# Kernel tuning notes

Measured on AMD Instinct MI355X. Metric: run time of the kernel, lower is better.

The kernel has to match this reference:

```python
import jax, jax.numpy as jnp
import numpy as np

DIM = 512
HEADS = 8
DH = DIM // HEADS  # 64

def setup_inputs() -> dict:
    key = jax.random.key(0)
    ks = jax.random.split(key, 10)
    s = 1.0 / np.sqrt(DIM)
    return {
        "x": jax.random.normal(ks[0], (8, 4096, DIM), dtype=jnp.float32),
        "x_d": jax.random.normal(ks[1], (8, 4096, DIM), dtype=jnp.float32),
        "W_qkv_rgb": jax.random.normal(ks[2], (DIM, 3 * DIM), dtype=jnp.float32) * s,
        "W_qkv_T": jax.random.normal(ks[3], (DIM, 3 * DIM), dtype=jnp.float32) * s,
        "temperature_rgb": jnp.ones((HEADS, 1, 1), dtype=jnp.float32),
        "temperature_T": jnp.ones((HEADS, 1, 1), dtype=jnp.float32),
        "W_proj_rgb": jax.random.normal(ks[4], (DIM, DIM), dtype=jnp.float32) * s,
        "b_proj_rgb": jnp.zeros((DIM,), dtype=jnp.float32),
        "W_proj_T": jax.random.normal(ks[5], (DIM, DIM), dtype=jnp.float32) * s,
        "b_proj_T": jnp.zeros((DIM,), dtype=jnp.float32),
    }

def _split_qkv(t, W):
    # t: (B,N,C) -> q,k,v each (B,H,d,N)  (channels-as-tokens layout)
    B, N, C = t.shape
    qkv = (t @ W).reshape(B, N, 3, HEADS, DH)
    qkv = qkv.transpose(2, 0, 3, 4, 1)  # (3,B,H,d,N)
    return qkv[0], qkv[1], qkv[2]

def _l2norm(a):
    # normalize over last axis (token dim N), matching F.normalize eps=1e-12
    n = jnp.sqrt(jnp.sum(a * a, axis=-1, keepdims=True))
    return a / jnp.maximum(n, 1e-12)

def _xca(q, k, v, temp):
    # q,k,v: (B,H,d,N); temp: (H,1,1) -> out (B,N,C)
    attn = jnp.einsum("bhdn,bhen->bhde", q, k) * temp  # (B,H,d,d)
    attn = jax.nn.softmax(attn, axis=-1)
    out = jnp.einsum("bhde,bhen->bhdn", attn, v)  # (B,H,d,N)
    B = out.shape[0]
    N = out.shape[-1]
    return out.transpose(0, 3, 1, 2).reshape(B, N, HEADS * DH)

def reference(x, x_d, W_qkv_rgb, W_qkv_T, temperature_rgb, temperature_T,
              W_proj_rgb, b_proj_rgb, W_proj_T, b_proj_T):
    q_rgb, k_rgb, v_rgb = _split_qkv(x, W_qkv_rgb)
    q_T, k_T, v_T = _split_qkv(x_d, W_qkv_T)
    q_rgb = _l2norm(q_rgb); k_rgb = _l2norm(k_rgb)
    q_T = _l2norm(q_T); k_T = _l2norm(k_T)
    out_rgb = _xca(q_rgb, k_T, v_T, temperature_rgb)
    out_T = _xca(q_T, k_rgb, v_rgb, temperature_T)
    out_rgb = out_rgb @ W_proj_rgb + b_proj_rgb
    out_T = out_T @ W_proj_T + b_proj_T
    return out_rgb, out_T
```

## Files before the change

kernel.cpp:

```cpp
#include <hip/hip_runtime.h>
#include <hip/hip_bf16.h>
#include <math.h>
#include <stdint.h>

typedef __bf16 bf16;
typedef __bf16 bf16x8 __attribute__((ext_vector_type(8)));
typedef float  floatx4 __attribute__((ext_vector_type(4)));

#define HEADS 8
#define DH    64
#define NB    8
#define NTOK  4096
#define CDIM  512
#define MTOT  32768
#define PART_STRIDE 16777216L

__device__ __forceinline__ void gload16(const bf16* g, bf16* l) {
    __builtin_amdgcn_global_load_lds(
        (const __attribute__((address_space(1))) unsigned int*)g,
        (__attribute__((address_space(3))) unsigned int*)l,
        16, 0, 0);
}

__global__ void detect_kernel(const bf16* __restrict__ w, int* __restrict__ flag)
{
    __shared__ int cnt[256];
    int c = 0;
    for (int i = 0; i < 64; ++i) {
        float v = fabsf((float)w[threadIdx.x + i * 256]);
        if (v > 1e3f) c++;
    }
    cnt[threadIdx.x] = c;
    __syncthreads();
    if (threadIdx.x == 0) {
        int s = 0;
        for (int i = 0; i < 256; ++i) s += cnt[i];
        *flag = (s > 500) ? 1 : 0;
    }
}

__global__ void misc_kernel(const void* t0, const void* t1, const void* b0, const void* b1,
                            const int* __restrict__ flag, float* __restrict__ misc)
{
    bool f32 = (*flag != 0);
    int tid = threadIdx.x;
    #define RD(p, i) (f32 ? ((const float*)(p))[i] : (float)((const bf16*)(p))[i])
    if (tid < 8) { misc[tid] = RD(t0, tid); misc[8 + tid] = RD(t1, tid); }
    for (int i = tid; i < 512; i += 256) {
        misc[16 + i]  = RD(b0, i);
        misc[528 + i] = RD(b1, i);
    }
    #undef RD
}

__global__ void wt_kernel(const void* __restrict__ W, bf16* __restrict__ Wt, int K, int N,
                          const int* __restrict__ flag)
{
    int idx = blockIdx.x * 256 + threadIdx.x;
    if (idx >= K * N) return;
    bool f32 = (*flag != 0);
    int n = idx / K;
    int k = idx - n * K;
    float v = f32 ? ((const float*)W)[k * N + n] : (float)((const bf16*)W)[k * N + n];
    Wt[idx] = (bf16)v;
}

__global__ void cast_kernel(const void* __restrict__ X, bf16* __restrict__ Y,
                            const int* __restrict__ flag)
{
    size_t i = ((size_t)blockIdx.x * 256 + threadIdx.x) * 8;
    if (*flag) {
        const float* xf = (const float*)X + i;
        float4 a = *(const float4*)xf;
        float4 b = *(const float4*)(xf + 4);
        bf16 t[8] = {(bf16)a.x, (bf16)a.y, (bf16)a.z, (bf16)a.w,
                     (bf16)b.x, (bf16)b.y, (bf16)b.z, (bf16)b.w};
        *(uint4*)(Y + i) = *(uint4*)t;
    } else {
        *(uint4*)(Y + i) = *(const uint4*)((const bf16*)X + i);
    }
}

__global__ __launch_bounds__(512, 2) void gemm_bt(
    const bf16* __restrict__ A, const bf16* __restrict__ Bt,
    const float* __restrict__ bias, void* __restrict__ C, bf16* __restrict__ Cv,
    long c_base, const int* __restrict__ cflag)
{
    __shared__ bf16 lds[2][2][2][128 * 64];

    const int tid  = threadIdx.x;
    const int lane = tid & 63;
    const int w    = tid >> 6;
    const int wmi  = w >> 2;
    const int wni  = w & 3;
    const int l15  = lane & 15;
    const int quad = lane >> 4;

    const int m0 = blockIdx.x * 256;
    const int n0 = blockIdx.y * 256;

    const int rl0 = w * 16 + (lane >> 3);
    const int swz = ((lane & 7) ^ (rl0 & 7)) * 8;
    const bf16* Abase = A  + (size_t)(m0 + rl0) * 512 + swz;
    const bf16* Bbase = Bt + (size_t)(n0 + rl0) * 512 + swz;
    const int ldst0 = w * 1024;

    const int rxor  = l15 & 7;
    const int k0off = (quad ^ rxor) * 8;
    const int k1off = ((4 + quad) ^ rxor) * 8;
    const bf16* Ah0 = &lds[0][0][wmi][l15 * 64];
    const bf16* Ah1 = &lds[1][0][wmi][l15 * 64];
    const bf16* Bh0 = &lds[0][1][wni >> 1][((wni & 1) * 64 + l15) * 64];
    const bf16* Bh1 = &lds[1][1][wni >> 1][((wni & 1) * 64 + l15) * 64];

    bf16x8 aR[4][2], bR[4][2];
    floatx4 acc[8][4] = {};

#define STAGE_A(b, h, t) do { \
    const bf16* _g = Abase + (h) * 65536 + (t) * 64; \
    gload16(_g,        &lds[b][0][h][ldst0]); \
    gload16(_g + 4096, &lds[b][0][h][ldst0 + 512]); \
} while (0)
#define STAGE_B(b, h, t) do { \
    const bf16* _g = Bbase + (h) * 65536 + (t) * 64; \
    gload16(_g,        &lds[b][1][h][ldst0]); \
    gload16(_g + 4096, &lds[b][1][h][ldst0 + 512]); \
} while (0)
#define RD_A(b, qm) do { \
    _Pragma("unroll") for (int _i = 0; _i < 4; ++_i) { \
        aR[_i][0] = *(const bf16x8*)(Ah##b + ((qm) * 4 + _i) * 1024 + k0off); \
        aR[_i][1] = *(const bf16x8*)(Ah##b + ((qm) * 4 + _i) * 1024 + k1off); \
    } \
} while (0)
#define RD_B(b, qn) do { \
    _Pragma("unroll") for (int _j = 0; _j < 2; ++_j) { \
        bR[(qn) * 2 + _j][0] = *(const bf16x8*)(Bh##b + ((qn) * 2 + _j) * 1024 + k0off); \
        bR[(qn) * 2 + _j][1] = *(const bf16x8*)(Bh##b + ((qn) * 2 + _j) * 1024 + k1off); \
    } \
} while (0)
#define MM(qm, qn) do { \
    _Pragma("unroll") for (int _i = 0; _i < 4; ++_i) \
    _Pragma("unroll") for (int _j = 0; _j < 2; ++_j) { \
        acc[(qm)*4+_i][(qn)*2+_j] = __builtin_amdgcn_mfma_f32_16x16x32_bf16( \
            aR[_i][0], bR[(qn)*2+_j][0], acc[(qm)*4+_i][(qn)*2+_j], 0, 0, 0); \
        acc[(qm)*4+_i][(qn)*2+_j] = __builtin_amdgcn_mfma_f32_16x16x32_bf16( \
            aR[_i][1], bR[(qn)*2+_j][1], acc[(qm)*4+_i][(qn)*2+_j], 0, 0, 0); \
    } \
} while (0)
#define SYNC   asm volatile("s_barrier" ::: "memory")
#define VMW(n) asm volatile("s_waitcnt vmcnt(" #n ")" ::: "memory")
#define PRIO1  __builtin_amdgcn_s_setprio(1)
#define PRIO0  __builtin_amdgcn_s_setprio(0)

#define TILE(t, b, nb, W) do { \
     \
    RD_A(b, 0); RD_B(b, 0); \
    if ((t) + 1 < 8) STAGE_B(nb, 1, (t) + 1); \
    SYNC; PRIO1; MM(0, 0); PRIO0; SYNC; \
     \
    RD_B(b, 1); \
    if ((t) + 1 < 8) STAGE_A(nb, 1, (t) + 1); \
    SYNC; PRIO1; MM(0, 1); PRIO0; SYNC; \
     \
    RD_A(b, 1); \
    if ((t) + 2 < 8) STAGE_B(b, 0, (t) + 2); \
    SYNC; PRIO1; MM(1, 1); PRIO0; SYNC; \
     \
    if ((t) + 2 < 8) STAGE_A(b, 0, (t) + 2); \
    SYNC; PRIO1; MM(1, 0); PRIO0; \
    VMW(W); SYNC; \
} while (0)

    STAGE_A(0, 0, 0); STAGE_A(0, 1, 0); STAGE_B(0, 0, 0); STAGE_B(0, 1, 0);
    STAGE_B(1, 0, 1); STAGE_A(1, 0, 1);
    VMW(4);
    SYNC;

    TILE(0, 0, 1, 4);
    TILE(1, 1, 0, 4);
    TILE(2, 0, 1, 4);
    TILE(3, 1, 0, 4);
    TILE(4, 0, 1, 4);
    TILE(5, 1, 0, 4);
    TILE(6, 0, 1, 0);
    TILE(7, 1, 0, 0);

#undef TILE
#undef STAGE_A
#undef STAGE_B
#undef RD_A
#undef RD_B
#undef MM
#undef SYNC
#undef VMW
#undef PRIO1
#undef PRIO0

    const bool cf32 = cflag && (*cflag != 0);
    const int  part = n0 >> 9;
    const long rowB = (long)m0 + wmi * 128 + quad * 4;
    const int  colB = (n0 & 511) + wni * 64 + l15;

    float bv[4];
    #pragma unroll
    for (int fj = 0; fj < 4; ++fj)
        bv[fj] = bias ? bias[n0 + wni * 64 + fj * 16 + l15] : 0.0f;

    if (part == 2) {
        #pragma unroll
        for (int fi = 0; fi < 8; ++fi)
            #pragma unroll
            for (int rr = 0; rr < 4; ++rr) {
                bf16* op = Cv + (rowB + fi * 16 + rr) * CDIM + colB;
                #pragma unroll
                for (int fj = 0; fj < 4; ++fj)
                    op[fj * 16] = (bf16)acc[fi][fj][rr];
            }
    } else if (cf32) {
        float* Cp = (float*)C + c_base + (long)part * PART_STRIDE;
        #pragma unroll
        for (int fi = 0; fi < 8; ++fi)
            #pragma unroll
            for (int rr = 0; rr < 4; ++rr) {
                float* op = Cp + (rowB + fi * 16 + rr) * CDIM + colB;
                #pragma unroll
                for (int fj = 0; fj < 4; ++fj)
                    op[fj * 16] = acc[fi][fj][rr] + bv[fj];
            }
    } else {
        bf16* Cp = (bf16*)C + c_base + (long)part * PART_STRIDE;
        #pragma unroll
        for (int fi = 0; fi < 8; ++fi)
            #pragma unroll
            for (int rr = 0; rr < 4; ++rr) {
                bf16* op = Cp + (rowB + fi * 16 + rr) * CDIM + colB;
                #pragma unroll
                for (int fj = 0; fj < 4; ++fj)
                    op[fj * 16] = (bf16)(acc[fi][fj][rr] + bv[fj]);
            }
    }
}

__global__ __launch_bounds__(256) void xca_gk(
    const bf16* __restrict__ Q0, const bf16* __restrict__ K0,
    const bf16* __restrict__ Q1, const bf16* __restrict__ K1,
    float* __restrict__ G, float* __restrict__ NQ, float* __restrict__ NK)
{
    __shared__ bf16 Tq[64 * 72];
    __shared__ bf16 Tk[64 * 72];

    int bid = blockIdx.x;
    int nq4 = bid & 3;
    int h   = (bid >> 2) & 7;
    int b   = (bid >> 5) & 7;
    int s   = bid >> 8;
    int sbh = s * 64 + b * 8 + h;

    const bf16* qsrc = s ? Q1 : Q0;
    const bf16* ksrc = s ? K0 : K1;

    int tid  = threadIdx.x;
    int lane = tid & 63;
    int wv   = tid >> 6;
    int wr   = wv >> 1;
    int wc   = wv & 1;
    int l15  = lane & 15;
    int quad = lane >> 4;
    bool isQ = (wv == 0 || wv == 3);

    int m_thr = tid & 7;
    int d0    = m_thr * 8;
    int u     = tid >> 3;
    int u_w   = u ^ (m_thr << 2);
    int wbase = d0 * 72 + 2 * u_w;

    int aoff[2][2], boff[2][2];
    #pragma unroll
    for (int i = 0; i < 2; ++i) {
        int ra = wr * 32 + i * 16 + l15;
        int rb = wc * 32 + i * 16 + l15;
        #pragma unroll
        for (int ss = 0; ss < 2; ++ss) {
            int ulog = ss * 16 + quad * 4;
            aoff[i][ss] = ra * 72 + 2 * (ulog ^ ((ra >> 3) << 2));
            boff[i][ss] = rb * 72 + 2 * (ulog ^ ((rb >> 3) << 2));
        }
    }

    long gbase = (long)(b * NTOK + nq4 * 1024) * CDIM + h * DH + d0;
    const bf16* qg = qsrc + gbase;
    const bf16* kg = ksrc + gbase;

    floatx4 accG[2][2] = {};
    floatx4 accN[2] = {};

    uint4 qA, qB, kA, kB;
    {
        size_t off = (size_t)(2 * u) * CDIM;
        qA = *(const uint4*)(qg + off);
        qB = *(const uint4*)(qg + off + CDIM);
        kA = *(const uint4*)(kg + off);
        kB = *(const uint4*)(kg + off + CDIM);
    }

    for (int t = 0; t < 16; ++t) {
        __syncthreads();
        {
            const unsigned short* pa = (const unsigned short*)&qA;
            const unsigned short* pb = (const unsigned short*)&qB;
            const unsigned short* pc = (const unsigned short*)&kA;
            const unsigned short* pd = (const unsigned short*)&kB;
            #pragma unroll
            for (int j = 0; j < 8; ++j) {
                *(uint32_t*)((char*)Tq + (size_t)(wbase + j * 72) * 2) =
                    (uint32_t)pa[j] | ((uint32_t)pb[j] << 16);
                *(uint32_t*)((char*)Tk + (size_t)(wbase + j * 72) * 2) =
                    (uint32_t)pc[j] | ((uint32_t)pd[j] << 16);
            }
        }
        __syncthreads();
        if (t + 1 < 16) {
            size_t off = (size_t)((t + 1) * 64 + 2 * u) * CDIM;
            qA = *(const uint4*)(qg + off);
            qB = *(const uint4*)(qg + off + CDIM);
            kA = *(const uint4*)(kg + off);
            kB = *(const uint4*)(kg + off + CDIM);
        }
        #pragma unroll
        for (int ss = 0; ss < 2; ++ss) {
            bf16x8 a0 = *(const bf16x8*)&Tq[aoff[0][ss]];
            bf16x8 a1 = *(const bf16x8*)&Tq[aoff[1][ss]];
            bf16x8 b0 = *(const bf16x8*)&Tk[boff[0][ss]];
            bf16x8 b1 = *(const bf16x8*)&Tk[boff[1][ss]];
            accG[0][0] = __builtin_amdgcn_mfma_f32_16x16x32_bf16(a0, b0, accG[0][0], 0, 0, 0);
            accG[0][1] = __builtin_amdgcn_mfma_f32_16x16x32_bf16(a0, b1, accG[0][1], 0, 0, 0);
            accG[1][0] = __builtin_amdgcn_mfma_f32_16x16x32_bf16(a1, b0, accG[1][0], 0, 0, 0);
            accG[1][1] = __builtin_amdgcn_mfma_f32_16x16x32_bf16(a1, b1, accG[1][1], 0, 0, 0);
            if (isQ) {
                accN[0] = __builtin_amdgcn_mfma_f32_16x16x32_bf16(a0, a0, accN[0], 0, 0, 0);
                accN[1] = __builtin_amdgcn_mfma_f32_16x16x32_bf16(a1, a1, accN[1], 0, 0, 0);
            } else {
                accN[0] = __builtin_amdgcn_mfma_f32_16x16x32_bf16(b0, b0, accN[0], 0, 0, 0);
                accN[1] = __builtin_amdgcn_mfma_f32_16x16x32_bf16(b1, b1, accN[1], 0, 0, 0);
            }
        }
    }

    float* Gp = G + (size_t)sbh * 4096;
    #pragma unroll
    for (int i = 0; i < 2; ++i)
        #pragma unroll
        for (int j = 0; j < 2; ++j)
            #pragma unroll
            for (int rr = 0; rr < 4; ++rr)
                atomicAdd(&Gp[(wr * 32 + i * 16 + quad * 4 + rr) * 64 + wc * 32 + j * 16 + l15],
                          accG[i][j][rr]);

    float* Np  = isQ ? NQ : NK;
    int nbase  = (isQ ? wr : wc) * 32;
    if ((l15 >> 2) == quad) {
        atomicAdd(&Np[(size_t)sbh * 64 + nbase + l15],      accN[0][l15 & 3]);
        atomicAdd(&Np[(size_t)sbh * 64 + nbase + 16 + l15], accN[1][l15 & 3]);
    }
}

__global__ void xca_soft(const float* __restrict__ G,
                         const float* __restrict__ NQ, const float* __restrict__ NK,
                         const float* __restrict__ misc, bf16* __restrict__ P)
{
    int sbh = blockIdx.x;
    int s = sbh >> 6;
    int h = sbh & 7;
    int d = threadIdx.x;

    __shared__ float rk[64];
    rk[d] = 1.0f / fmaxf(sqrtf(NK[sbh * 64 + d]), 1e-12f);
    __syncthreads();

    float rq = 1.0f / fmaxf(sqrtf(NQ[sbh * 64 + d]), 1e-12f);
    float t  = misc[s * 8 + h];
    const float* Gr = G + (sbh * 64 + d) * 64;

    float a[64];
    float mx = -1e30f;
    #pragma unroll
    for (int e = 0; e < 64; ++e) {
        a[e] = Gr[e] * rq * rk[e] * t;
        mx = fmaxf(mx, a[e]);
    }
    float sum = 0.f;
    #pragma unroll
    for (int e = 0; e < 64; ++e) { a[e] = expf(a[e] - mx); sum += a[e]; }
    float inv = 1.0f / sum;
    bf16* Pr = P + (sbh * 64 + d) * 64;
    #pragma unroll
    for (int e = 0; e < 64; ++e) Pr[e] = (bf16)(a[e] * inv);
}

__global__ __launch_bounds__(256) void xca_pv(
    const bf16* __restrict__ V0, const bf16* __restrict__ V1,
    const bf16* __restrict__ P, bf16* __restrict__ xca)
{
    int bid = blockIdx.x;
    int nq4 = bid & 3;
    int h   = (bid >> 2) & 7;
    int b   = (bid >> 5) & 7;
    int s   = bid >> 8;
    int sbh = s * 64 + b * 8 + h;

    const bf16* vsrc = s ? V0 : V1;

    int tid = threadIdx.x;
    int lane = tid & 63;
    int wave = tid >> 6;
    int l15 = lane & 15;
    int quad = lane >> 4;

    const bf16* Pb = P + sbh * 4096;
    bf16x8 pf[4][2];
    #pragma unroll
    for (int i = 0; i < 4; ++i)
        #pragma unroll
        for (int h2 = 0; h2 < 2; ++h2)
            pf[i][h2] = *(const bf16x8*)&Pb[(i * 16 + l15) * 64 + h2 * 32 + quad * 8];

    int n_start = nq4 * 1024 + wave * 256;
    for (int nt = 0; nt < 16; ++nt) {
        int nb = n_start + nt * 16;
        const bf16* vp = vsrc + (long)(b * NTOK + nb + l15) * CDIM + h * DH + quad * 8;
        bf16x8 v0 = *(const bf16x8*)vp;
        bf16x8 v1 = *(const bf16x8*)(vp + 32);
        floatx4 acc[4] = {};
        #pragma unroll
        for (int i = 0; i < 4; ++i) {
            acc[i] = __builtin_amdgcn_mfma_f32_16x16x32_bf16(v0, pf[i][0], acc[i], 0, 0, 0);
            acc[i] = __builtin_amdgcn_mfma_f32_16x16x32_bf16(v1, pf[i][1], acc[i], 0, 0, 0);
        }
        bf16* op = xca + (long)((s * NB + b) * NTOK + nb + quad * 4) * CDIM + h * DH + l15;
        #pragma unroll
        for (int i = 0; i < 4; ++i)
            #pragma unroll
            for (int r = 0; r < 4; ++r)
                op[(long)r * CDIM + i * 16] = (bf16)acc[i][r];
    }
}

extern "C" void kernel_launch(void* const* d_in, const int* in_sizes, int n_in,
                              void* d_out, int out_size, void* d_ws, size_t ws_size,
                              hipStream_t stream)
{
    const void* x     = d_in[0];
    const void* x_d   = d_in[1];
    const void* Wq0   = d_in[2];
    const void* Wq1   = d_in[3];
    const void* temp0 = d_in[4];
    const void* temp1 = d_in[5];
    const void* Wp0   = d_in[6];
    const void* bp0   = d_in[7];
    const void* Wp1   = d_in[8];
    const void* bp1   = d_in[9];

    char* ws = (char*)d_ws;
    bf16*  Q0   = (bf16*)(ws);
    bf16*  K0   = (bf16*)(ws + 33554432);
    bf16*  Q1   = (bf16*)(ws + 67108864);
    bf16*  K1   = (bf16*)(ws + 100663296);
    bf16*  Xb0  = (bf16*)(ws + 134217728);
    bf16*  Xb1  = (bf16*)(ws + 167772160);
    bf16*  xca  = (bf16*)(ws + 134217728);
    bf16*  wtq0 = (bf16*)(ws + 201326592);
    bf16*  wtq1 = (bf16*)(ws + 202899456);
    bf16*  wtp0 = (bf16*)(ws + 204472320);
    bf16*  wtp1 = (bf16*)(ws + 204996608);
    float* G    = (float*)(ws + 205520896);
    float* NQ   = (float*)(ws + 207618048);
    float* NK   = (float*)(ws + 207650816);
    bf16*  P    = (bf16*)(ws + 207683584);
    int*   flag = (int*)(ws + 208732160);
    float* misc = (float*)(ws + 208732224);

    bf16* V0 = (bf16*)d_out;
    bf16* V1 = (bf16*)d_out + PART_STRIDE;

    hipMemsetAsync(ws + 205520896, 0, 2162688, stream);

    detect_kernel<<<1, 256, 0, stream>>>((const bf16*)Wq0, flag);
    misc_kernel<<<1, 256, 0, stream>>>(temp0, temp1, bp0, bp1, flag, misc);

    wt_kernel<<<(512 * 1536 + 255) / 256, 256, 0, stream>>>(Wq0, wtq0, 512, 1536, flag);
    wt_kernel<<<(512 * 1536 + 255) / 256, 256, 0, stream>>>(Wq1, wtq1, 512, 1536, flag);
    wt_kernel<<<(512 * 512 + 255) / 256, 256, 0, stream>>>(Wp0, wtp0, 512, 512, flag);
    wt_kernel<<<(512 * 512 + 255) / 256, 256, 0, stream>>>(Wp1, wtp1, 512, 512, flag);

    cast_kernel<<<8192, 256, 0, stream>>>(x,   Xb0, flag);
    cast_kernel<<<8192, 256, 0, stream>>>(x_d, Xb1, flag);

    gemm_bt<<<dim3(128, 6), 512, 0, stream>>>(Xb0, wtq0, nullptr, Q0, V0, 0L, nullptr);
    gemm_bt<<<dim3(128, 6), 512, 0, stream>>>(Xb1, wtq1, nullptr, Q1, V1, 0L, nullptr);

    xca_gk<<<512, 256, 0, stream>>>(Q0, K0, Q1, K1, G, NQ, NK);
    xca_soft<<<128, 64, 0, stream>>>(G, NQ, NK, misc, P);
    xca_pv<<<512, 256, 0, stream>>>(V0, V1, P, xca);

    gemm_bt<<<dim3(128, 2), 512, 0, stream>>>(xca,               wtp0, misc + 16,  d_out, nullptr, 0L,          flag);
    gemm_bt<<<dim3(128, 2), 512, 0, stream>>>(xca + PART_STRIDE, wtp1, misc + 528, d_out, nullptr, PART_STRIDE, flag);
}
```

Before: 528.9 us.

## Merge small prep kernels, batch GEMM launches, and stage epilogues through LDS

Folds the weight-transpose and misc kernels into one prep kernel and the two cast launches into one, cutting launch count. Each QKV GEMM launch becomes one z-batched launch in which a block loops over three N-tiles and overlaps the previous tile's epilogue with the next tile's loads. GEMM and PV epilogues now stage results in swizzled LDS so global stores are 16-byte and coalesced instead of scattered 2-byte writes. The trade-offs are fewer blocks in flight for the QKV GEMM, and reuse of the operand-staging LDS as epilogue scratch, which could race if the waits are wrong.

```diff
diff --git a/kernel.cpp b/kernel.cpp
--- a/kernel.cpp
+++ b/kernel.cpp
@@ -39,36 +39,47 @@
     }
 }
 
-__global__ void misc_kernel(const void* t0, const void* t1, const void* b0, const void* b1,
-                            const int* __restrict__ flag, float* __restrict__ misc)
-{
-    bool f32 = (*flag != 0);
-    int tid = threadIdx.x;
-    #define RD(p, i) (f32 ? ((const float*)(p))[i] : (float)((const bf16*)(p))[i])
-    if (tid < 8) { misc[tid] = RD(t0, tid); misc[8 + tid] = RD(t1, tid); }
-    for (int i = tid; i < 512; i += 256) {
-        misc[16 + i]  = RD(b0, i);
-        misc[528 + i] = RD(b1, i);
-    }
-    #undef RD
-}
-
-__global__ void wt_kernel(const void* __restrict__ W, bf16* __restrict__ Wt, int K, int N,
-                          const int* __restrict__ flag)
-{
-    int idx = blockIdx.x * 256 + threadIdx.x;
+__device__ __forceinline__ void wt_body(const void* __restrict__ W, bf16* __restrict__ Wt,
+                                        int K, int N, bool f32, int idx)
+{
     if (idx >= K * N) return;
-    bool f32 = (*flag != 0);
     int n = idx / K;
     int k = idx - n * K;
     float v = f32 ? ((const float*)W)[k * N + n] : (float)((const bf16*)W)[k * N + n];
     Wt[idx] = (bf16)v;
 }
 
-__global__ void cast_kernel(const void* __restrict__ X, bf16* __restrict__ Y,
+__global__ void prep_kernel(const void* Wq0, const void* Wq1, const void* Wp0, const void* Wp1,
+                            const void* t0, const void* t1, const void* b0, const void* b1,
+                            const int* __restrict__ flag, float* __restrict__ misc,
+                            bf16* wtq0, bf16* wtq1, bf16* wtp0, bf16* wtp1)
+{
+    bool f32 = (*flag != 0);
+    int blk = blockIdx.x;
+    int tid = threadIdx.x;
+    if (blk < 3072)      wt_body(Wq0, wtq0, 512, 1536, f32, blk * 256 + tid);
+    else if (blk < 6144) wt_body(Wq1, wtq1, 512, 1536, f32, (blk - 3072) * 256 + tid);
+    else if (blk < 7168) wt_body(Wp0, wtp0, 512, 512, f32, (blk - 6144) * 256 + tid);
+    else if (blk < 8192) wt_body(Wp1, wtp1, 512, 512, f32, (blk - 7168) * 256 + tid);
+    else {
+        #define RD(p, i) (f32 ? ((const float*)(p))[i] : (float)((const bf16*)(p))[i])
+        if (tid < 8) { misc[tid] = RD(t0, tid); misc[8 + tid] = RD(t1, tid); }
+        for (int i = tid; i < 512; i += 256) {
+            misc[16 + i]  = RD(b0, i);
+            misc[528 + i] = RD(b1, i);
+        }
+        #undef RD
+    }
+}
+
+__global__ void cast_kernel(const void* __restrict__ X0, const void* __restrict__ X1,
+                            bf16* __restrict__ Y0, bf16* __restrict__ Y1,
                             const int* __restrict__ flag)
 {
-    size_t i = ((size_t)blockIdx.x * 256 + threadIdx.x) * 8;
+    int blk = blockIdx.x;
+    const void* X = (blk < 8192) ? X0 : X1;
+    bf16* Y       = (blk < 8192) ? Y0 : Y1;
+    size_t i = ((size_t)(blk & 8191) * 256 + threadIdx.x) * 8;
     if (*flag) {
         const float* xf = (const float*)X + i;
         float4 a = *(const float4*)xf;
@@ -81,12 +92,22 @@
     }
 }
 
+template<int NJOBS>
 __global__ __launch_bounds__(512, 2) void gemm_bt(
-    const bf16* __restrict__ A, const bf16* __restrict__ Bt,
-    const float* __restrict__ bias, void* __restrict__ C, bf16* __restrict__ Cv,
-    long c_base, const int* __restrict__ cflag)
+    const bf16* __restrict__ A0, const bf16* __restrict__ A1,
+    const bf16* __restrict__ Bt0, const bf16* __restrict__ Bt1,
+    const float* __restrict__ bias0, const float* __restrict__ bias1,
+    void* __restrict__ C, bf16* __restrict__ Cv0, bf16* __restrict__ Cv1,
+    long cbase0, long cbase1, const int* __restrict__ cflag)
 {
     __shared__ bf16 lds[2][2][2][128 * 64];
+
+    const int z = blockIdx.z;
+    const bf16* A    = z ? A1 : A0;
+    const bf16* Btz  = z ? Bt1 : Bt0;
+    const float* bias = z ? bias1 : bias0;
+    bf16* Cvz        = z ? Cv1 : Cv0;
+    const long c_base = z ? cbase1 : cbase0;
 
     const int tid  = threadIdx.x;
     const int lane = tid & 63;
@@ -97,12 +118,11 @@
     const int quad = lane >> 4;
 
     const int m0 = blockIdx.x * 256;
-    const int n0 = blockIdx.y * 256;
 
     const int rl0 = w * 16 + (lane >> 3);
     const int swz = ((lane & 7) ^ (rl0 & 7)) * 8;
-    const bf16* Abase = A  + (size_t)(m0 + rl0) * 512 + swz;
-    const bf16* Bbase = Bt + (size_t)(n0 + rl0) * 512 + swz;
+    const bf16* Abase = A + (size_t)(m0 + rl0) * 512 + swz;
+    const bf16* Bbase = nullptr;
     const int ldst0 = w * 1024;
 
     const int rxor  = l15 & 7;
@@ -112,6 +132,8 @@
     const bf16* Ah1 = &lds[1][0][wmi][l15 * 64];
     const bf16* Bh0 = &lds[0][1][wni >> 1][((wni & 1) * 64 + l15) * 64];
     const bf16* Bh1 = &lds[1][1][wni >> 1][((wni & 1) * 64 + l15) * 64];
+
+    bf16* eb = (bf16*)lds + ((w < 4) ? (5 * 8192 + w * 2048) : (7 * 8192 + (w - 4) * 2048));
 
     bf16x8 aR[4][2], bR[4][2];
     floatx4 acc[8][4] = {};
@@ -153,37 +175,100 @@
 #define PRIO0  __builtin_amdgcn_s_setprio(0)
 
 #define TILE(t, b, nb, W) do { \
-     \
     RD_A(b, 0); RD_B(b, 0); \
     if ((t) + 1 < 8) STAGE_B(nb, 1, (t) + 1); \
     SYNC; PRIO1; MM(0, 0); PRIO0; SYNC; \
-     \
     RD_B(b, 1); \
     if ((t) + 1 < 8) STAGE_A(nb, 1, (t) + 1); \
     SYNC; PRIO1; MM(0, 1); PRIO0; SYNC; \
-     \
     RD_A(b, 1); \
     if ((t) + 2 < 8) STAGE_B(b, 0, (t) + 2); \
     SYNC; PRIO1; MM(1, 1); PRIO0; SYNC; \
-     \
     if ((t) + 2 < 8) STAGE_A(b, 0, (t) + 2); \
     SYNC; PRIO1; MM(1, 0); PRIO0; \
     VMW(W); SYNC; \
 } while (0)
 
-    STAGE_A(0, 0, 0); STAGE_A(0, 1, 0); STAGE_B(0, 0, 0); STAGE_B(0, 1, 0);
-    STAGE_B(1, 0, 1); STAGE_A(1, 0, 1);
-    VMW(4);
-    SYNC;
-
-    TILE(0, 0, 1, 4);
-    TILE(1, 1, 0, 4);
-    TILE(2, 0, 1, 4);
-    TILE(3, 1, 0, 4);
-    TILE(4, 0, 1, 4);
-    TILE(5, 1, 0, 4);
-    TILE(6, 0, 1, 0);
-    TILE(7, 1, 0, 0);
+#define EPI_BF16(DST, PN0, BV) do { \
+    bf16* _dp = (DST) + (size_t)(m0 + wmi * 128) * CDIM + ((PN0) & 511) + wni * 64; \
+    _Pragma("unroll") for (int _p = 0; _p < 4; ++_p) { \
+        _Pragma("unroll") for (int _f2 = 0; _f2 < 2; ++_f2) \
+        _Pragma("unroll") for (int _fj = 0; _fj < 4; ++_fj) \
+        _Pragma("unroll") for (int _rr = 0; _rr < 4; ++_rr) { \
+            int _r32 = _f2 * 16 + quad * 4 + _rr; \
+            int _cs  = (_fj * 16 + l15) ^ (((_r32 >> 2) & 3) << 4); \
+            eb[_r32 * 64 + _cs] = (bf16)(acc[_p * 2 + _f2][_fj][_rr] + BV[_fj]); \
+        } \
+        _Pragma("unroll") for (int _q = 0; _q < 4; ++_q) { \
+            int _rl = _q * 8 + (lane >> 3); \
+            int _c8 = ((lane & 7) * 8) ^ (((_rl >> 2) & 3) << 4); \
+            uint4 _vv = *(const uint4*)&eb[_rl * 64 + _c8]; \
+            *(uint4*)(_dp + (size_t)(_p * 32 + _rl) * CDIM + (lane & 7) * 8) = _vv; \
+        } \
+    } \
+    _Pragma("unroll") for (int _i = 0; _i < 8; ++_i) \
+    _Pragma("unroll") for (int _j = 0; _j < 4; ++_j) acc[_i][_j] = (floatx4){0,0,0,0}; \
+} while (0)
+
+    float bz[4] = {0.f, 0.f, 0.f, 0.f};
+    int prev_n0 = 0;
+
+    for (int j = 0; j < NJOBS; ++j) {
+        const int n0 = (blockIdx.y * NJOBS + j) * 256;
+        Bbase = Btz + (size_t)(n0 + rl0) * 512 + swz;
+
+        STAGE_A(0, 0, 0); STAGE_A(0, 1, 0); STAGE_B(0, 0, 0); STAGE_B(0, 1, 0);
+        STAGE_B(1, 0, 1); STAGE_A(1, 0, 1);
+
+        if (j > 0) {
+            int pp = prev_n0 >> 9;
+            bf16* dst = (pp == 2) ? Cvz : ((bf16*)C + c_base + (long)pp * PART_STRIDE);
+            EPI_BF16(dst, prev_n0, bz);
+            VMW(18);
+        } else {
+            VMW(4);
+        }
+        SYNC;
+
+        TILE(0, 0, 1, 4);
+        TILE(1, 1, 0, 4);
+        TILE(2, 0, 1, 4);
+        TILE(3, 1, 0, 4);
+        TILE(4, 0, 1, 4);
+        TILE(5, 1, 0, 4);
+        TILE(6, 0, 1, 0);
+        TILE(7, 1, 0, 0);
+
+        prev_n0 = n0;
+    }
+
+    const bool cf32 = cflag && (*cflag != 0);
+    const int  part = prev_n0 >> 9;
+    if (!cf32) {
+        float bv[4];
+        #pragma unroll
+        for (int fj = 0; fj < 4; ++fj)
+            bv[fj] = bias ? bias[prev_n0 + wni * 64 + fj * 16 + l15] : 0.0f;
+        bf16* dst = (part == 2) ? Cvz : ((bf16*)C + c_base + (long)part * PART_STRIDE);
+        EPI_BF16(dst, prev_n0, bv);
+    } else {
+        const long rowB = (long)m0 + wmi * 128 + quad * 4;
+        const int  colB = (prev_n0 & 511) + wni * 64 + l15;
+        float bv[4];
+        #pragma unroll
+        for (int fj = 0; fj < 4; ++fj)
+            bv[fj] = bias ? bias[prev_n0 + wni * 64 + fj * 16 + l15] : 0.0f;
+        float* Cp = (float*)C + c_base + (long)part * PART_STRIDE;
+        #pragma unroll
+        for (int fi = 0; fi < 8; ++fi)
+            #pragma unroll
+            for (int rr = 0; rr < 4; ++rr) {
+                float* op = Cp + (rowB + fi * 16 + rr) * CDIM + colB;
+                #pragma unroll
+                for (int fj = 0; fj < 4; ++fj)
+                    op[fj * 16] = acc[fi][fj][rr] + bv[fj];
+            }
+    }
 
 #undef TILE
 #undef STAGE_A
@@ -195,50 +280,7 @@
 #undef VMW
 #undef PRIO1
 #undef PRIO0
-
-    const bool cf32 = cflag && (*cflag != 0);
-    const int  part = n0 >> 9;
-    const long rowB = (long)m0 + wmi * 128 + quad * 4;
-    const int  colB = (n0 & 511) + wni * 64 + l15;
-
-    float bv[4];
-    #pragma unroll
-    for (int fj = 0; fj < 4; ++fj)
-        bv[fj] = bias ? bias[n0 + wni * 64 + fj * 16 + l15] : 0.0f;
-
-    if (part == 2) {
-        #pragma unroll
-        for (int fi = 0; fi < 8; ++fi)
-            #pragma unroll
-            for (int rr = 0; rr < 4; ++rr) {
-                bf16* op = Cv + (rowB + fi * 16 + rr) * CDIM + colB;
-                #pragma unroll
-                for (int fj = 0; fj < 4; ++fj)
-                    op[fj * 16] = (bf16)acc[fi][fj][rr];
-            }
-    } else if (cf32) {
-        float* Cp = (float*)C + c_base + (long)part * PART_STRIDE;
-        #pragma unroll
-        for (int fi = 0; fi < 8; ++fi)
-            #pragma unroll
-            for (int rr = 0; rr < 4; ++rr) {
-                float* op = Cp + (rowB + fi * 16 + rr) * CDIM + colB;
-                #pragma unroll
-                for (int fj = 0; fj < 4; ++fj)
-                    op[fj * 16] = acc[fi][fj][rr] + bv[fj];
-            }
-    } else {
-        bf16* Cp = (bf16*)C + c_base + (long)part * PART_STRIDE;
-        #pragma unroll
-        for (int fi = 0; fi < 8; ++fi)
-            #pragma unroll
-            for (int rr = 0; rr < 4; ++rr) {
-                bf16* op = Cp + (rowB + fi * 16 + rr) * CDIM + colB;
-                #pragma unroll
-                for (int fj = 0; fj < 4; ++fj)
-                    op[fj * 16] = (bf16)(acc[fi][fj][rr] + bv[fj]);
-            }
-    }
+#undef EPI_BF16
 }
 
 __global__ __launch_bounds__(256) void xca_gk(
@@ -401,6 +443,8 @@
     const bf16* __restrict__ V0, const bf16* __restrict__ V1,
     const bf16* __restrict__ P, bf16* __restrict__ xca)
 {
+    __shared__ bf16 pvs[4 * 1024];
+
     int bid = blockIdx.x;
     int nq4 = bid & 3;
     int h   = (bid >> 2) & 7;
@@ -415,6 +459,8 @@
     int wave = tid >> 6;
     int l15 = lane & 15;
     int quad = lane >> 4;
+
+    bf16* eb = pvs + wave * 1024;
 
     const bf16* Pb = P + sbh * 4096;
     bf16x8 pf[4][2];
@@ -436,12 +482,22 @@
             acc[i] = __builtin_amdgcn_mfma_f32_16x16x32_bf16(v0, pf[i][0], acc[i], 0, 0, 0);
             acc[i] = __builtin_amdgcn_mfma_f32_16x16x32_bf16(v1, pf[i][1], acc[i], 0, 0, 0);
         }
-        bf16* op = xca + (long)((s * NB + b) * NTOK + nb + quad * 4) * CDIM + h * DH + l15;
         #pragma unroll
         for (int i = 0; i < 4; ++i)
             #pragma unroll
-            for (int r = 0; r < 4; ++r)
-                op[(long)r * CDIM + i * 16] = (bf16)acc[i][r];
+            for (int r = 0; r < 4; ++r) {
+                int tk = quad * 4 + r;
+                int cs = (i * 16 + l15) ^ (((tk >> 2) & 3) << 4);
+                eb[tk * 64 + cs] = (bf16)acc[i][r];
+            }
+        bf16* ob = xca + (long)((s * NB + b) * NTOK + nb) * CDIM + h * DH;
+        #pragma unroll
+        for (int p = 0; p < 2; ++p) {
+            int tk = p * 8 + (lane >> 3);
+            int c8 = ((lane & 7) * 8) ^ (((tk >> 2) & 3) << 4);
+            uint4 vv = *(const uint4*)&eb[tk * 64 + c8];
+            *(uint4*)(ob + (size_t)tk * CDIM + (lane & 7) * 8) = vv;
+        }
     }
 }
 
@@ -485,23 +541,19 @@
     hipMemsetAsync(ws + 205520896, 0, 2162688, stream);
 
     detect_kernel<<<1, 256, 0, stream>>>((const bf16*)Wq0, flag);
-    misc_kernel<<<1, 256, 0, stream>>>(temp0, temp1, bp0, bp1, flag, misc);
-
-    wt_kernel<<<(512 * 1536 + 255) / 256, 256, 0, stream>>>(Wq0, wtq0, 512, 1536, flag);
-    wt_kernel<<<(512 * 1536 + 255) / 256, 256, 0, stream>>>(Wq1, wtq1, 512, 1536, flag);
-    wt_kernel<<<(512 * 512 + 255) / 256, 256, 0, stream>>>(Wp0, wtp0, 512, 512, flag);
-    wt_kernel<<<(512 * 512 + 255) / 256, 256, 0, stream>>>(Wp1, wtp1, 512, 512, flag);
-
-    cast_kernel<<<8192, 256, 0, stream>>>(x,   Xb0, flag);
-    cast_kernel<<<8192, 256, 0, stream>>>(x_d, Xb1, flag);
-
-    gemm_bt<<<dim3(128, 6), 512, 0, stream>>>(Xb0, wtq0, nullptr, Q0, V0, 0L, nullptr);
-    gemm_bt<<<dim3(128, 6), 512, 0, stream>>>(Xb1, wtq1, nullptr, Q1, V1, 0L, nullptr);
+    prep_kernel<<<8193, 256, 0, stream>>>(Wq0, Wq1, Wp0, Wp1, temp0, temp1, bp0, bp1,
+                                          flag, misc, wtq0, wtq1, wtp0, wtp1);
+    cast_kernel<<<16384, 256, 0, stream>>>(x, x_d, Xb0, Xb1, flag);
+
+    gemm_bt<3><<<dim3(128, 2, 2), 512, 0, stream>>>(
+        Xb0, Xb1, wtq0, wtq1, nullptr, nullptr,
+        (void*)ws, V0, V1, 0L, 2L * PART_STRIDE, nullptr);
 
     xca_gk<<<512, 256, 0, stream>>>(Q0, K0, Q1, K1, G, NQ, NK);
     xca_soft<<<128, 64, 0, stream>>>(G, NQ, NK, misc, P);
     xca_pv<<<512, 256, 0, stream>>>(V0, V1, P, xca);
 
-    gemm_bt<<<dim3(128, 2), 512, 0, stream>>>(xca,               wtp0, misc + 16,  d_out, nullptr, 0L,          flag);
-    gemm_bt<<<dim3(128, 2), 512, 0, stream>>>(xca + PART_STRIDE, wtp1, misc + 528, d_out, nullptr, PART_STRIDE, flag);
-}
+    gemm_bt<1><<<dim3(128, 2, 2), 512, 0, stream>>>(
+        xca, xca + PART_STRIDE, wtp0, wtp1, misc + 16, misc + 528,
+        d_out, nullptr, nullptr, 0L, PART_STRIDE, flag);
+}
```

New measurement: 621.0 us. +17.4%, slower.
